# Optimization experiments

Measured on AMD Instinct MI355X. Metric: run time of the kernel, lower is better.

## Reference

```python
import jax, jax.numpy as jnp
import numpy as np

E_NUM, R_NUM, D, B = 100000, 200, 128, 4096


def setup_inputs() -> dict:
    key = jax.random.key(0)
    k = jax.random.split(key, 7)
    return {
        "h": jax.random.randint(k[0], (B,), 0, E_NUM),
        "r": jax.random.randint(k[1], (B,), 0, R_NUM),
        "pos_t": jax.random.randint(k[2], (B,), 0, E_NUM),
        "neg_t": jax.random.randint(k[3], (B,), 0, E_NUM),
        # xavier-normal-ish init scales
        "entity_embed": jax.random.normal(k[4], (E_NUM, D), jnp.float32) * 0.12,
        "relation_embed": jax.random.normal(k[5], (R_NUM, D), jnp.float32) * 0.12,
        "trans_M": jax.random.normal(k[6], (R_NUM, D * D), jnp.float32) * 0.011,
    }


def reference(h, r, pos_t, neg_t, entity_embed, relation_embed, trans_M):
    h_e = entity_embed[h]            # [B, D]
    pos_e = entity_embed[pos_t]      # [B, D]
    neg_e = entity_embed[neg_t]      # [B, D]
    r_e = relation_embed[r]          # [B, D]
    W_r = trans_M[r].reshape(-1, D, D)  # [B, D, D]
    # row-vector @ matrix per sample: (1xD) @ (DxD) -> D
    trans_h = jnp.einsum("bd,bde->be", h_e, W_r)
    trans_pos = jnp.einsum("bd,bde->be", pos_e, W_r)
    trans_neg = jnp.einsum("bd,bde->be", neg_e, W_r)
    return (trans_h, r_e, trans_pos, trans_neg)
```

## Files before the change

### kernel.cpp

```cpp
#include <hip/hip_runtime.h>

#define DDIM    128
#define NS      4
#define SG      2
#define SCOL    32
#define SCH     10
#define MROWS   32
#define XSTRIDE 136
#define WSTRIDE 136
#define SEGCAP  96

typedef __attribute__((ext_vector_type(8))) short bf16x8;
typedef __attribute__((ext_vector_type(4))) float f32x4;

static __device__ inline unsigned short f2b(float f) {
    unsigned u = __float_as_uint(f);
    u += 0x7fff + ((u >> 16) & 1);
    return (unsigned short)(u >> 16);
}

__global__ __launch_bounds__(256) void transr_mfma(
    const int* __restrict__ h, const int* __restrict__ r,
    const int* __restrict__ pos_t, const int* __restrict__ neg_t,
    const float* __restrict__ ent, const float* __restrict__ rel,
    const float* __restrict__ M, float* __restrict__ out,
    int B, int R)
{
    const int bid  = blockIdx.x;
    const int rb   = bid % R;
    const int rest = bid / R;
    const int qc   = rest & (NS - 1);
    const int sg   = rest >> 2;
    const int t    = threadIdx.x;
    const int wvid = t >> 6;
    const int ln   = t & 63;

    __shared__ __align__(16) unsigned short Xl[MROWS * XSTRIDE];
    __shared__ __align__(16) unsigned short Wt[SCOL  * WSTRIDE];
    __shared__ int seg[4][SEGCAP];
    __shared__ int wcnt[4];
    __shared__ int list_s[4 * SEGCAP];

    const int g  = t >> 4;
    const int nl = t & 15;
    const float* __restrict__ Wg = M + (size_t)rb * DDIM * DDIM + qc * SCOL;
    float wreg0[8], wreg1[8];
    #pragma unroll
    for (int j = 0; j < 8; ++j) wreg0[j] = Wg[(size_t)(g * 8 + j) * DDIM + nl];
    #pragma unroll
    for (int j = 0; j < 8; ++j) wreg1[j] = Wg[(size_t)(g * 8 + j) * DDIM + nl + 16];

    int segn = 0;
    const int qlen4  = B >> 4;
    const int qbase4 = wvid * qlen4;
    const int4* __restrict__ r4 = (const int4*)r;
    for (int i0 = 0; i0 < qlen4; i0 += 64) {
        const int  e4 = qbase4 + i0 + ln;
        const int4 rv = r4[e4];
        const int  ib = e4 << 2;
        #pragma unroll
        for (int j = 0; j < 4; ++j) {
            const int  rj = (j == 0) ? rv.x : (j == 1) ? rv.y : (j == 2) ? rv.z : rv.w;
            const bool f  = (rj == rb);
            const unsigned long long m = __ballot(f);
            if (f) {
                const int p = segn + __popcll(m & ((1ull << ln) - 1ull));
                if (p < SEGCAP) seg[wvid][p] = ib + j;
            }
            segn += __popcll(m);
        }
    }
    if (ln == 0) wcnt[wvid] = min(segn, SEGCAP);

    {
        bf16x8 w0, w1;
        #pragma unroll
        for (int j = 0; j < 8; ++j) { w0[j] = (short)f2b(wreg0[j]); w1[j] = (short)f2b(wreg1[j]); }
        *(bf16x8*)(&Wt[nl * WSTRIDE + g * 8])        = w0;
        *(bf16x8*)(&Wt[(nl + 16) * WSTRIDE + g * 8]) = w1;
    }
    __syncthreads();

    const int c0 = wcnt[0], c1 = wcnt[1], c2 = wcnt[2], c3 = wcnt[3];
    const int cum1 = c0, cum2 = c0 + c1, cum3 = c0 + c1 + c2;
    const int cnt  = cum3 + c3;
    if (cnt == 0) return;

    for (int lin = t; lin < cnt; lin += 256) {
        int w, k;
        if      (lin < cum1) { w = 0; k = lin;        }
        else if (lin < cum2) { w = 1; k = lin - cum1; }
        else if (lin < cum3) { w = 2; k = lin - cum2; }
        else                 { w = 3; k = lin - cum3; }
        list_s[lin] = seg[w][k];
    }
    __syncthreads();

    const int halfc  = (cnt + 1) >> 1;
    const int gstart = sg * halfc;
    const int gcnt   = max(0, min(cnt - gstart, halfc));

    if (sg == 0) {
        for (int lin = t; lin < cnt * (SCOL / 4); lin += 256) {
            const int j  = lin >> 3;
            const int c4 = lin & 7;
            const float4 v = *(const float4*)(rel + (size_t)rb * DDIM + qc * SCOL + c4 * 4);
            *(float4*)(out + (size_t)B * DDIM + (size_t)list_s[j] * DDIM + qc * SCOL + c4 * 4) = v;
        }
    }
    if (gcnt == 0) return;

    const int lr = ln & 15;
    const int lg = ln >> 4;
    const int mt = wvid & 1;
    const int nt = wvid >> 1;
    bf16x8 bfr[4];
    #pragma unroll
    for (int ks = 0; ks < 4; ++ks) {
        const int kg = ks * 4 + lg;
        bfr[ks] = *(const bf16x8*)(&Wt[(nt * 16 + lr) * WSTRIDE + kg * 8]);
    }

    const size_t BD = (size_t)B * DDIM;
    for (int ch = 0; ch < gcnt; ch += SCH) {
        const int ccnt = min(SCH, gcnt - ch);
        const int rows_valid = 3 * ccnt;

        for (int lin = t; lin < rows_valid * 16; lin += 256) {
            const int row  = lin >> 4;
            const int kg   = lin & 15;
            const int jj   = row / 3;
            const int v    = row - 3 * jj;
            const int sidx = list_s[gstart + ch + jj];
            const int eid  = (v == 0) ? h[sidx] : (v == 1) ? pos_t[sidx] : neg_t[sidx];
            const float4 a = *(const float4*)(ent + (size_t)eid * DDIM + kg * 8);
            const float4 b = *(const float4*)(ent + (size_t)eid * DDIM + kg * 8 + 4);
            bf16x8 x;
            x[0] = (short)f2b(a.x); x[1] = (short)f2b(a.y);
            x[2] = (short)f2b(a.z); x[3] = (short)f2b(a.w);
            x[4] = (short)f2b(b.x); x[5] = (short)f2b(b.y);
            x[6] = (short)f2b(b.z); x[7] = (short)f2b(b.w);
            *(bf16x8*)(&Xl[row * XSTRIDE + kg * 8]) = x;
        }
        __syncthreads();

        f32x4 acc = {0.f, 0.f, 0.f, 0.f};
        #pragma unroll
        for (int ks = 0; ks < 4; ++ks) {
            const int kg = ks * 4 + lg;
            const bf16x8 a = *(const bf16x8*)(&Xl[(mt * 16 + lr) * XSTRIDE + kg * 8]);
            acc = __builtin_amdgcn_mfma_f32_16x16x32_bf16(a, bfr[ks], acc, 0, 0, 0);
        }

        #pragma unroll
        for (int q = 0; q < 4; ++q) {
            const int rowe = mt * 16 + lg * 4 + q;
            if (rowe < rows_valid) {
                const int jj = rowe / 3;
                const int v2 = rowe - 3 * jj;
                const size_t s = (size_t)list_s[gstart + ch + jj];
                float* bp = (v2 == 0) ? out : (v2 == 1) ? (out + 2 * BD) : (out + 3 * BD);
                bp[s * DDIM + qc * SCOL + nt * 16 + lr] = acc[q];
            }
        }
        __syncthreads();
    }
}

extern "C" void kernel_launch(void* const* d_in, const int* in_sizes, int n_in,
                              void* d_out, int out_size, void* d_ws, size_t ws_size,
                              hipStream_t stream) {
    const int*   h     = (const int*)d_in[0];
    const int*   r     = (const int*)d_in[1];
    const int*   pos_t = (const int*)d_in[2];
    const int*   neg_t = (const int*)d_in[3];
    const float* ent   = (const float*)d_in[4];
    const float* rel   = (const float*)d_in[5];
    const float* M     = (const float*)d_in[6];
    float*       out   = (float*)d_out;

    const int B = in_sizes[0];
    const int R = in_sizes[5] / DDIM;

    transr_mfma<<<dim3(R * NS * SG), dim3(256), 0, stream>>>(
        h, r, pos_t, neg_t, ent, rel, M, out, B, R);
}
```

Before: 15.48 us.

## Load entity rows directly into MFMA A-fragments, drop LDS staging and chunk barriers

Entity ids for all matched samples are now resolved once into a shared eid table. Each wave then gathers its 16-row A fragments straight from global memory into registers, converting to bf16 in place. This removes the Xl LDS staging buffer and the two per-chunk __syncthreads. SEGCAP also drops from 96 to 64, which shrinks shared memory but truncates any relation whose per-wave match count exceeds 64 (expected count is about 5).

Measured after the change: 21.09 us. 36.2% more time.

```diff
diff --git a/kernel.cpp b/kernel.cpp
--- a/kernel.cpp
+++ b/kernel.cpp
@@ -4,11 +4,8 @@
 #define NS      4
 #define SG      2
 #define SCOL    32
-#define SCH     10
-#define MROWS   32
-#define XSTRIDE 136
 #define WSTRIDE 136
-#define SEGCAP  96
+#define SEGCAP  64
 
 typedef __attribute__((ext_vector_type(8))) short bf16x8;
 typedef __attribute__((ext_vector_type(4))) float f32x4;
@@ -35,11 +32,11 @@
     const int wvid = t >> 6;
     const int ln   = t & 63;
 
-    __shared__ __align__(16) unsigned short Xl[MROWS * XSTRIDE];
-    __shared__ __align__(16) unsigned short Wt[SCOL  * WSTRIDE];
+    __shared__ __align__(16) unsigned short Wt[SCOL * WSTRIDE];
     __shared__ int seg[4][SEGCAP];
     __shared__ int wcnt[4];
     __shared__ int list_s[4 * SEGCAP];
+    __shared__ int eid_s[3 * 4 * SEGCAP];
 
     const int g  = t >> 4;
     const int nl = t & 15;
@@ -96,9 +93,12 @@
     }
     __syncthreads();
 
-    const int halfc  = (cnt + 1) >> 1;
-    const int gstart = sg * halfc;
-    const int gcnt   = max(0, min(cnt - gstart, halfc));
+    for (int i = t; i < 3 * cnt; i += 256) {
+        const int jj = i / 3;
+        const int v  = i - 3 * jj;
+        const int sidx = list_s[jj];
+        eid_s[i] = (v == 0) ? h[sidx] : (v == 1) ? pos_t[sidx] : neg_t[sidx];
+    }
 
     if (sg == 0) {
         for (int lin = t; lin < cnt * (SCOL / 4); lin += 256) {
@@ -108,7 +108,14 @@
             *(float4*)(out + (size_t)B * DDIM + (size_t)list_s[j] * DDIM + qc * SCOL + c4 * 4) = v;
         }
     }
+    __syncthreads();
+
+    const int halfc  = (cnt + 1) >> 1;
+    const int gstart = sg * halfc;
+    const int gcnt   = max(0, min(cnt - gstart, halfc));
     if (gcnt == 0) return;
+    const int rows_base = 3 * gstart;
+    const int nrows     = 3 * gcnt;
 
     const int lr = ln & 15;
     const int lg = ln >> 4;
@@ -122,48 +129,37 @@
     }
 
     const size_t BD = (size_t)B * DDIM;
-    for (int ch = 0; ch < gcnt; ch += SCH) {
-        const int ccnt = min(SCH, gcnt - ch);
-        const int rows_valid = 3 * ccnt;
-
-        for (int lin = t; lin < rows_valid * 16; lin += 256) {
-            const int row  = lin >> 4;
-            const int kg   = lin & 15;
-            const int jj   = row / 3;
-            const int v    = row - 3 * jj;
-            const int sidx = list_s[gstart + ch + jj];
-            const int eid  = (v == 0) ? h[sidx] : (v == 1) ? pos_t[sidx] : neg_t[sidx];
-            const float4 a = *(const float4*)(ent + (size_t)eid * DDIM + kg * 8);
-            const float4 b = *(const float4*)(ent + (size_t)eid * DDIM + kg * 8 + 4);
-            bf16x8 x;
-            x[0] = (short)f2b(a.x); x[1] = (short)f2b(a.y);
-            x[2] = (short)f2b(a.z); x[3] = (short)f2b(a.w);
-            x[4] = (short)f2b(b.x); x[5] = (short)f2b(b.y);
-            x[6] = (short)f2b(b.z); x[7] = (short)f2b(b.w);
-            *(bf16x8*)(&Xl[row * XSTRIDE + kg * 8]) = x;
-        }
-        __syncthreads();
+    for (int m0 = mt * 16; m0 < nrows; m0 += 32) {
+        const int rowl = min(m0 + lr, nrows - 1);
+        const int eid  = eid_s[rows_base + rowl];
+        const float* __restrict__ xr = ent + (size_t)eid * DDIM;
 
         f32x4 acc = {0.f, 0.f, 0.f, 0.f};
         #pragma unroll
         for (int ks = 0; ks < 4; ++ks) {
             const int kg = ks * 4 + lg;
-            const bf16x8 a = *(const bf16x8*)(&Xl[(mt * 16 + lr) * XSTRIDE + kg * 8]);
-            acc = __builtin_amdgcn_mfma_f32_16x16x32_bf16(a, bfr[ks], acc, 0, 0, 0);
+            const float4 a = *(const float4*)(xr + kg * 8);
+            const float4 b = *(const float4*)(xr + kg * 8 + 4);
+            bf16x8 af;
+            af[0] = (short)f2b(a.x); af[1] = (short)f2b(a.y);
+            af[2] = (short)f2b(a.z); af[3] = (short)f2b(a.w);
+            af[4] = (short)f2b(b.x); af[5] = (short)f2b(b.y);
+            af[6] = (short)f2b(b.z); af[7] = (short)f2b(b.w);
+            acc = __builtin_amdgcn_mfma_f32_16x16x32_bf16(af, bfr[ks], acc, 0, 0, 0);
         }
 
         #pragma unroll
         for (int q = 0; q < 4; ++q) {
-            const int rowe = mt * 16 + lg * 4 + q;
-            if (rowe < rows_valid) {
-                const int jj = rowe / 3;
-                const int v2 = rowe - 3 * jj;
-                const size_t s = (size_t)list_s[gstart + ch + jj];
+            const int rowe = m0 + lg * 4 + q;
+            if (rowe < nrows) {
+                const int rg = rows_base + rowe;
+                const int jj = rg / 3;
+                const int v2 = rg - 3 * jj;
+                const size_t s = (size_t)list_s[jj];
                 float* bp = (v2 == 0) ? out : (v2 == 1) ? (out + 2 * BD) : (out + 3 * BD);
                 bp[s * DDIM + qc * SCOL + nt * 16 + lr] = acc[q];
             }
         }
-        __syncthreads();
     }
 }
 
```
